# Kernel optimization log

Measured on AMD Instinct MI355X. Metric: run time of the kernel, lower is better.

## Reference

```python
import jax, jax.numpy as jnp
import numpy as np
from jax import lax
from jax.scipy.ndimage import map_coordinates

L = 10  # unrolled iterations (LayerNo)


def _conv(x, w, b):
    # x [N,C,H,W], w [O,I,3,3] -> 'SAME' padding == padding=1 for k=3
    y = lax.conv_general_dilated(x, w, (1, 1), 'SAME',
                                 dimension_numbers=('NCHW', 'OIHW', 'NCHW'))
    return y + b[None, :, None, None]


def _prelu(x, a):
    return jnp.where(x >= 0, x, a * x)


def _block(x, w1, b1, a1, w2, b2, a2, w3, b3):
    x = _prelu(_conv(x, w1, b1), a1)
    x = _prelu(_conv(x, w2, b2), a2)
    return _conv(x, w3, b3)


def _radon_forward(img, theta, det_count):
    # img [S,S]; parallel-beam line integrals -> [A, det_count]
    S = img.shape[0]
    c = (S - 1) / 2.0
    s = jnp.arange(det_count, dtype=img.dtype) - (det_count - 1) / 2.0
    t = jnp.arange(S, dtype=img.dtype) - (S - 1) / 2.0

    def one(a):
        ca, sa = jnp.cos(a), jnp.sin(a)
        x = s[:, None] * ca - t[None, :] * sa  # [D,S] sample cols
        y = s[:, None] * sa + t[None, :] * ca  # [D,S] sample rows
        vals = map_coordinates(img, [y + c, x + c], order=1, mode='constant', cval=0.0)
        return vals.sum(axis=1)

    return jax.vmap(one)(theta)


def _radon_backprojection(sino, theta, S):
    # sino [A,D] -> [S,S] (adjoint smear with bilinear detector interpolation)
    A, D = sino.shape
    c = (S - 1) / 2.0
    dc = (D - 1) / 2.0
    ax = jnp.arange(S, dtype=sino.dtype) - c
    Y, X = jnp.meshgrid(ax, ax, indexing='ij')  # row=y, col=x

    def one(row, a):
        ca, sa = jnp.cos(a), jnp.sin(a)
        sidx = (X * ca + Y * sa + dc).ravel()
        return map_coordinates(row, [sidx], order=1, mode='constant', cval=0.0).reshape(S, S)

    return jax.vmap(one)(sino, theta).sum(axis=0)


def _filter_sinogram(sino):
    # Ram-Lak ramp filter along detector axis with FBP normalization pi/(2*A)
    A, D = sino.shape
    n = 2048  # next power of two >= 2*D (D=729)
    F = jnp.fft.rfft(sino, n=n, axis=-1)
    ramp = (2.0 * jnp.fft.rfftfreq(n)).astype(sino.dtype)
    out = jnp.fft.irfft(F * ramp, n=n, axis=-1)[..., :D]
    return out * (jnp.pi / (2.0 * A))


def _forward(cond, x0, g, theta, theta_label,
             dw1, db1, da1, dw2, db2, da2, dw3, db3,
             pw1, pb1, pa1, pw2, pb2, pa2, pw3, pb3):
    S = x0.shape[2]
    A, D = g.shape[2], g.shape[3]
    h = jnp.zeros((1, 5, A, D), dtype=g.dtype)
    f = jnp.zeros((1, 5, S, S), dtype=g.dtype)
    for i in range(L):
        Op_f = _radon_forward(f[0, 1], theta, D)[None, None]          # [1,1,A,D]
        h = h + _block(jnp.concatenate([h, Op_f, g], axis=1),
                       dw1[i], db1[i], da1[i], dw2[i], db2[i], da2[i], dw3[i], db3[i])
        h1 = _filter_sinogram(h[0, 0])                                 # [A,D]
        OpAdj_h = _radon_backprojection(h1, theta, S)[None, None]      # [1,1,S,S]
        f = f + _block(jnp.concatenate([f, OpAdj_h], axis=1),
                       pw1[i], pb1[i], pa1[i], pw2[i], pb2[i], pa2[i], pw3[i], pb3[i])
    return (f[:, 0:1], f[:, 0:1], f[:, 0:1])


def setup_inputs() -> dict:
    key = jax.random.key(0)
    ks = jax.random.split(key, 12)
    S, A, D = 512, 60, 729

    def xavier(k, shp):
        cout, cin = shp[1], shp[2]
        std = np.sqrt(2.0 / ((cin + cout) * 9.0)).astype(np.float32)
        return jax.random.normal(k, shp, dtype=jnp.float32) * std

    ang = jnp.linspace(0.0, np.pi, A, endpoint=False).astype(jnp.float32)
    return {
        'cond': jax.random.normal(ks[0], (1, 1, S, S), dtype=jnp.float32),
        'x0': jax.random.normal(ks[1], (1, 1, S, S), dtype=jnp.float32),
        'g': jax.random.normal(ks[2], (1, 1, A, D), dtype=jnp.float32),
        'theta': ang,
        'theta_label': ang,
        'dw1': xavier(ks[3], (L, 32, 7, 3, 3)), 'db1': jnp.zeros((L, 32), jnp.float32), 'da1': 0.25 * jnp.ones((L,), jnp.float32),
        'dw2': xavier(ks[4], (L, 32, 32, 3, 3)), 'db2': jnp.zeros((L, 32), jnp.float32), 'da2': 0.25 * jnp.ones((L,), jnp.float32),
        'dw3': xavier(ks[5], (L, 5, 32, 3, 3)), 'db3': jnp.zeros((L, 5), jnp.float32),
        'pw1': xavier(ks[6], (L, 32, 6, 3, 3)), 'pb1': jnp.zeros((L, 32), jnp.float32), 'pa1': 0.25 * jnp.ones((L,), jnp.float32),
        'pw2': xavier(ks[7], (L, 32, 32, 3, 3)), 'pb2': jnp.zeros((L, 32), jnp.float32), 'pa2': 0.25 * jnp.ones((L,), jnp.float32),
        'pw3': xavier(ks[8], (L, 5, 32, 3, 3)), 'pb3': jnp.zeros((L, 5), jnp.float32),
    }


def reference(cond, x0, g, theta, theta_label,
              dw1, db1, da1, dw2, db2, da2, dw3, db3,
              pw1, pb1, pa1, pw2, pb2, pa2, pw3, pb3):
    return _forward(cond, x0, g, theta, theta_label,
                    dw1, db1, da1, dw2, db2, da2, dw3, db3,
                    pw1, pb1, pa1, pw2, pb2, pa2, pw3, pb3)
```

## Files before the change

### kernel.cpp

```cpp
#include <hip/hip_runtime.h>
#include <math.h>

#define SS 512
#define AANG 60
#define DDET 729
#define NPIX (SS*SS)
#define NSIN (AANG*DDET)
#define NTAPS 1457
#define DRS 768

typedef float v4u __attribute__((ext_vector_type(4), aligned(4)));
typedef float v2u __attribute__((ext_vector_type(2), aligned(8)));
typedef short short8 __attribute__((ext_vector_type(8)));
typedef short short4v __attribute__((ext_vector_type(4)));
typedef float f32x4 __attribute__((ext_vector_type(4)));

__device__ inline unsigned short f2bf(float x){
  unsigned u = __float_as_uint(x);
  return (unsigned short)((u + 0x7fffu + ((u >> 16) & 1u)) >> 16);
}

__global__ void trig_kernel(const float* __restrict__ theta, float* __restrict__ trig){
  int a = threadIdx.x;
  if (a < AANG){ trig[a] = cosf(theta[a]); trig[AANG+a] = sinf(theta[a]); }
}

__global__ void taps_kernel(float* __restrict__ taps){
  __shared__ double red[256];
  int m  = blockIdx.x;
  int mm = m - 728;
  double s = 0.0;
  for (int k = 1 + (int)threadIdx.x; k <= 1023; k += 256){
    int phase = (k*mm) & 2047;
    s += (double)k * cos((double)phase * (M_PI/1024.0));
// ... 60 lines not shown
  float x = (t < 9 && j < Cin) ? w[(((size_t)(l*32+o)*Cin + j)*9) + t] : 0.f;
  unsigned short hb = f2bf(x);
  float hf = __uint_as_float((unsigned)hb << 16);
  unsigned short lb = f2bf(x - hf);
  size_t d = (size_t)l*6144 + (size_t)g*2048 + n*1024 + lane*8 + j;
  B[d]       = hb;
  B[d + 512] = lb;
}

__global__ void g_to_nhwc8(const float* __restrict__ g,
                           unsigned short* __restrict__ s8hi, unsigned short* __restrict__ s8lo){
  int idx = blockIdx.x*256 + (int)threadIdx.x;
  if (idx >= NSIN) return;
  int a = idx / DDET, d = idx - a*DDET;
  float x = g[idx];
  unsigned short hb = f2bf(x);
  float hf = __uint_as_float((unsigned)hb << 16);
  unsigned short lb = f2bf(x - hf);
  size_t p8 = ((size_t)(a+1)*DRS + d)*8 + 6;
  s8hi[p8] = hb;
  s8lo[p8] = lb;
}

__device__ inline void clipr(float al, float ial, float be, float lo, float hi,
                             float& A, float& B, bool& empty){
  if (fabsf(al) < 1e-7f){ if (be < lo || be > hi) empty = true; return; }
  float t0 = (lo - be)*ial, t1 = (hi - be)*ial;
  float mn = fminf(t0,t1), mx = fmaxf(t0,t1);
  A = fmaxf(A, mn); B = fminf(B, mx);
}

__device__ inline float samp_guard(const float* __restrict__ base, float aR, float bR,
                                   float aC, float bC, int t){
  float tp = (float)t - 255.5f;
  float R = fmaf(aR, tp, bR);
  float C = fmaf(aC, tp, bC);
// ... 55 lines not shown
        float tp = (float)t - 255.5f;
        float R = fmaf(aR, tp, bR);
        float C = fmaf(aC, tp, bC);
        int r0 = (int)R, c0 = (int)C;
        float fr = R - (float)r0, fc = C - (float)c0;
        const float* p = base + r0*SS + c0;
        float v00 = p[0], v01 = p[1], v10 = p[SS], v11 = p[SS+1];
        float top = v00 + fc*(v01-v00);
        float bot = v10 + fc*(v11-v10);
        acc += top + fr*(bot-top);
      }
    }
  }
  for (int off=32; off; off>>=1) acc += __shfl_down(acc, off);
  if (lane==0){
    unsigned short hb = f2bf(acc);
    float hf = __uint_as_float((unsigned)hb << 16);
    unsigned short lb = f2bf(acc - hf);
    size_t p8 = ((size_t)(a+1)*DRS + d)*8 + 5;
    s8hi[p8] = hb;
    s8lo[p8] = lb;
  }
}

__global__ __launch_bounds__(256) void filter_kernel2(
    const float* __restrict__ h0, const float* __restrict__ taps,
    float* __restrict__ h1){
  __shared__ float red[256];
  int a  = blockIdx.x / 12;
  int jb = blockIdx.x - a*12;
  int jl = (int)threadIdx.x & 63;
  int kq = (int)threadIdx.x >> 6;
  int j  = jb*64 + jl;
  float acc = 0.f;
  if (j < DDET){
    const float* row = h0 + a*DDET;
    const float* tp  = taps + 728 + j;
    int k0 = kq*183;
    int k1 = min(k0+183, DDET);
    for (int k=k0;k<k1;k++) acc = fmaf(row[k], tp[-k], acc);
  }
  red[threadIdx.x] = acc;
  __syncthreads();
  if ((int)threadIdx.x < 64 && j < DDET){
    float s = red[jl] + red[64+jl] + red[128+jl] + red[192+jl];
    h1[a*DDET + j] = s;
  }
}

__global__ __launch_bounds__(256) void backproj_kernel(
    const float* __restrict__ h1, const float* __restrict__ trig,
    unsigned short* __restrict__ hi8, unsigned short* __restrict__ lo8){
  __shared__ float sh[AANG*28];
  __shared__ int   sbase[AANG];
  __shared__ float strig[2*AANG];
  int tid = threadIdx.x;
  int x0 = (blockIdx.x & 31) * 16, y0 = (blockIdx.x >> 5) * 16;
  if (tid < 2*AANG) strig[tid] = trig[tid];
  __syncthreads();
  if (tid < AANG){
    float ca = strig[tid], sa = strig[AANG+tid];
// ... 11 lines not shown
    sh[s] = (idx >= 0 && idx < DDET) ? h1[a*DDET + idx] : 0.f;
  }
  __syncthreads();
  int x = x0 + (tid & 15), y = y0 + (tid >> 4);
  float X = (float)x - 255.5f, Y = (float)y - 255.5f;
  float acc = 0.f;
  #pragma unroll 6
  for (int a=0;a<AANG;a++){
    float sidx = fmaf(X, strig[a], fmaf(Y, strig[AANG+a], 364.0f));
    float ff = floorf(sidx);
    int k = (int)ff - sbase[a];
    float fi = sidx - ff;
    float v0 = sh[a*28+k], v1 = sh[a*28+k+1];
    acc += v0 + fi*(v1-v0);
  }
  unsigned short hb = f2bf(acc);
  float hf = __uint_as_float((unsigned)hb << 16);
  unsigned short lb = f2bf(acc - hf);
  size_t p8 = ((size_t)(y*SS + x))*8 + 5;
  hi8[p8] = hb;
  lo8[p8] = lb;
}

__global__ __launch_bounds__(64) void dual1_mfma(
    const unsigned short* __restrict__ hi8, const unsigned short* __restrict__ lo8,
    const unsigned short* __restrict__ Bimg1d,
    const float* __restrict__ bias, const float* __restrict__ prelu,
    unsigned short* __restrict__ outHi, unsigned short* __restrict__ outLo)
{
  __shared__ unsigned int tr[64][33];
  int y  = blockIdx.y;
  int lane = (int)threadIdx.x;
  int xw = blockIdx.x*64;
  int lm = lane & 15, lq = lane >> 4;
  f32x4 acc[4][2];
  #pragma unroll
  for (int s=0;s<4;s++){ acc[s][0] = (f32x4)0.f; acc[s][1] = (f32x4)0.f; }
  const short8* Bf = (const short8*)Bimg1d;
  #pragma unroll
  for (int g=0; g<3; g++){
    const short8* bp8 = Bf + g*256 + lane;
    short8 bh0 = bp8[0];
    short8 bl0 = bp8[64];
    short8 bh1 = bp8[128];
    short8 bl1 = bp8[192];
    int t = g*4 + lq; if (t > 8) t = 8;
    int dy = (t >= 6) ? 1 : ((t >= 3) ? 0 : -1);
    int dx = t - (dy+1)*3 - 1;
    int row = y + dy + 1;
    #pragma unroll
    for (int s=0; s<4; s++){
      int px = xw + s*16 + lm + dx;
      size_t off = (size_t)(row*DRS + px)*8;
      short8 ah = *(const short8*)(hi8 + off);
      short8 al = *(const short8*)(lo8 + off);
      acc[s][0] = __builtin_amdgcn_mfma_f32_16x16x32_bf16(ah, bh0, acc[s][0], 0,0,0);
      acc[s][1] = __builtin_amdgcn_mfma_f32_16x16x32_bf16(ah, bh1, acc[s][1], 0,0,0);
      acc[s][0] = __builtin_amdgcn_mfma_f32_16x16x32_bf16(al, bh0, acc[s][0], 0,0,0);
      acc[s][1] = __builtin_amdgcn_mfma_f32_16x16x32_bf16(al, bh1, acc[s][1], 0,0,0);
      acc[s][0] = __builtin_amdgcn_mfma_f32_16x16x32_bf16(ah, bl0, acc[s][0], 0,0,0);
      acc[s][1] = __builtin_amdgcn_mfma_f32_16x16x32_bf16(ah, bl1, acc[s][1], 0,0,0);
    }
  }
  float aa = *prelu;
  #pragma unroll
  for (int s=0;s<4;s++){
    #pragma unroll
    for (int n=0;n<2;n++){
      int o = n*16 + lm;
      float bv = bias[o];
      f32x4 v = acc[s][n];
      v.x+=bv; v.y+=bv; v.z+=bv; v.w+=bv;
      v.x=(v.x>=0.f)?v.x:aa*v.x; v.y=(v.y>=0.f)?v.y:aa*v.y;
      v.z=(v.z>=0.f)?v.z:aa*v.z; v.w=(v.w>=0.f)?v.w:aa*v.w;
      #pragma unroll
      for (int r=0;r<4;r++){
        float x = v[r];
        unsigned short hb = f2bf(x);
        float hf = __uint_as_float((unsigned)hb << 16);
        unsigned short lb = f2bf(x - hf);
        tr[s*16 + lq*4 + r][o] = ((unsigned)hb << 16) | (unsigned)lb;
      }
    }
  }
  __syncthreads();
  int c8 = lane & 3;
  int pxl = lane >> 2;
  #pragma unroll
  for (int k=0;k<4;k++){
    int px = pxl + k*16;
    int x = xw + px;
    if (x > 728) continue;
    short8 vh, vl;
    #pragma unroll
    for (int j=0;j<8;j++){
      unsigned p = tr[px][c8*8 + j];
      vh[j] = (short)(p >> 16);
      vl[j] = (short)(p & 0xffffu);
    }
    size_t base = ((size_t)(y+1)*DRS + x)*32 + c8*8;
    *(short8*)(outHi + base) = vh;
    *(short8*)(outLo + base) = vl;
  }
}

__global__ __launch_bounds__(64) void dual_mfma32(
    const unsigned short* __restrict__ hiB, const unsigned short* __restrict__ loB,
    const unsigned short* __restrict__ Bimg,
    const float* __restrict__ bias, const float* __restrict__ prelu,
    unsigned short* __restrict__ outHi, unsigned short* __restrict__ outLo)
{
  __shared__ unsigned int tr[64][33];
  int y  = blockIdx.y;
  int lane = (int)threadIdx.x;
  int xw = blockIdx.x*64;
  int lm = lane & 15, lq = lane >> 4;
  int laneoff = lm*32 + lq*8;
  f32x4 acc[4][2];
  #pragma unroll
  for (int s=0;s<4;s++){ acc[s][0] = (f32x4)0.f; acc[s][1] = (f32x4)0.f; }
  const short8* Bf = (const short8*)Bimg;
  #pragma unroll
  for (int dy=-1; dy<=1; dy++){
    const unsigned short* rh = hiB + (size_t)(y+dy+1)*DRS*32;
    const unsigned short* rl = loB + (size_t)(y+dy+1)*DRS*32;
    #pragma unroll
    for (int dx=-1; dx<=1; dx++){
      int tap = (dy+1)*3 + (dx+1);
      const short8* bp8 = Bf + tap*256 + lane;
      short8 bh0 = bp8[0];
      short8 bl0 = bp8[64];
      short8 bh1 = bp8[128];
      short8 bl1 = bp8[192];
      int xoff = (xw + dx)*32 + laneoff;
      #pragma unroll
      for (int s=0; s<4; s++){
        short8 ah = *(const short8*)(rh + xoff + s*512);
        short8 al = *(const short8*)(rl + xoff + s*512);
        acc[s][0] = __builtin_amdgcn_mfma_f32_16x16x32_bf16(ah, bh0, acc[s][0], 0,0,0);
        acc[s][1] = __builtin_amdgcn_mfma_f32_16x16x32_bf16(ah, bh1, acc[s][1], 0,0,0);
        acc[s][0] = __builtin_amdgcn_mfma_f32_16x16x32_bf16(al, bh0, acc[s][0], 0,0,0);
        acc[s][1] = __builtin_amdgcn_mfma_f32_16x16x32_bf16(al, bh1, acc[s][1], 0,0,0);
        acc[s][0] = __builtin_amdgcn_mfma_f32_16x16x32_bf16(ah, bl0, acc[s][0], 0,0,0);
        acc[s][1] = __builtin_amdgcn_mfma_f32_16x16x32_bf16(ah, bl1, acc[s][1], 0,0,0);
      }
    }
  }
  float aa = *prelu;
  #pragma unroll
  for (int s=0;s<4;s++){
    #pragma unroll
    for (int n=0;n<2;n++){
      int o = n*16 + lm;
      float bv = bias[o];
      f32x4 v = acc[s][n];
      v.x+=bv; v.y+=bv; v.z+=bv; v.w+=bv;
      v.x=(v.x>=0.f)?v.x:aa*v.x; v.y=(v.y>=0.f)?v.y:aa*v.y;
      v.z=(v.z>=0.f)?v.z:aa*v.z; v.w=(v.w>=0.f)?v.w:aa*v.w;
      #pragma unroll
      for (int r=0;r<4;r++){
        float x = v[r];
        unsigned short hb = f2bf(x);
        float hf = __uint_as_float((unsigned)hb << 16);
        unsigned short lb = f2bf(x - hf);
        tr[s*16 + lq*4 + r][o] = ((unsigned)hb << 16) | (unsigned)lb;
      }
    }
  }
  __syncthreads();
  int c8 = lane & 3;
  int pxl = lane >> 2;
  #pragma unroll
  for (int k=0;k<4;k++){
    int px = pxl + k*16;
    int x = xw + px;
    if (x > 728) continue;
    short8 vh, vl;
    #pragma unroll
    for (int j=0;j<8;j++){
      unsigned p = tr[px][c8*8 + j];
      vh[j] = (short)(p >> 16);
      vl[j] = (short)(p & 0xffffu);
    }
    size_t base = ((size_t)(y+1)*DRS + x)*32 + c8*8;
    *(short8*)(outHi + base) = vh;
    *(short8*)(outLo + base) = vl;
  }
}

__global__ __launch_bounds__(64) void dual3_mfma(
    const unsigned short* __restrict__ hiB, const unsigned short* __restrict__ loB,
    const unsigned short* __restrict__ Bimg3d,
    const float* __restrict__ bias,
    float* __restrict__ h,
    unsigned short* __restrict__ s8hi, unsigned short* __restrict__ s8lo)
{
  __shared__ unsigned int t8[64][6];
  int y  = blockIdx.y;
  int lane = (int)threadIdx.x;
  int xw = blockIdx.x*64;
  int lm = lane & 15, lq = lane >> 4;
  int laneoff = lm*32 + lq*8;
  f32x4 acc[4];
  #pragma unroll
  for (int s=0;s<4;s++) acc[s] = (f32x4)0.f;
  const short8* Bf = (const short8*)Bimg3d;
  #pragma unroll
  for (int dy=-1; dy<=1; dy++){
    const unsigned short* rh = hiB + (size_t)(y+dy+1)*DRS*32;
    const unsigned short* rl = loB + (size_t)(y+dy+1)*DRS*32;
    #pragma unroll
    for (int dx=-1; dx<=1; dx++){
      int tap = (dy+1)*3 + (dx+1);
      const short8* bp8 = Bf + tap*128 + lane;
      short8 bh = bp8[0];
      short8 bl = bp8[64];
      int xoff = (xw + dx)*32 + laneoff;
      #pragma unroll
      for (int s=0; s<4; s++){
        short8 ah = *(const short8*)(rh + xoff + s*512);
        short8 al = *(const short8*)(rl + xoff + s*512);
        acc[s] = __builtin_amdgcn_mfma_f32_16x16x32_bf16(ah, bh, acc[s], 0,0,0);
        acc[s] = __builtin_amdgcn_mfma_f32_16x16x32_bf16(al, bh, acc[s], 0,0,0);
        acc[s] = __builtin_amdgcn_mfma_f32_16x16x32_bf16(ah, bl, acc[s], 0,0,0);
      }
    }
  }
  if (lm < 5){
    float bv = bias[lm];
    #pragma unroll
    for (int s=0;s<4;s++){
      int px0 = xw + s*16 + lq*4;
      float* op = h + (size_t)lm*NSIN + y*DDET + px0;
      float nv0=0.f, nv1=0.f, nv2=0.f, nv3=0.f;
      if (px0 + 3 <= 728){
        v4u old = *(const v4u*)op;
        nv0 = old.x + acc[s].x + bv;
        nv1 = old.y + acc[s].y + bv;
        nv2 = old.z + acc[s].z + bv;
        nv3 = old.w + acc[s].w + bv;
        v4u st; st.x=nv0; st.y=nv1; st.z=nv2; st.w=nv3;
        *(v4u*)op = st;
      } else {
        if (px0   <= 728){ nv0 = op[0] + acc[s].x + bv; op[0] = nv0; }
        if (px0+1 <= 728){ nv1 = op[1] + acc[s].y + bv; op[1] = nv1; }
        if (px0+2 <= 728){ nv2 = op[2] + acc[s].z + bv; op[2] = nv2; }
        if (px0+3 <= 728){ nv3 = op[3] + acc[s].w + bv; op[3] = nv3; }
      }
      float nv[4] = {nv0,nv1,nv2,nv3};
      #pragma unroll
      for (int r=0;r<4;r++){
        float x = nv[r];
        unsigned short hb = f2bf(x);
        float hf = __uint_as_float((unsigned)hb << 16);
        unsigned short lb = f2bf(x - hf);
        t8[s*16 + lq*4 + r][lm] = ((unsigned)hb << 16) | (unsigned)lb;
      }
    }
  }
  __syncthreads();
  {
    int x = xw + lane;
    if (x <= 728){
      unsigned c0 = t8[lane][0], c1 = t8[lane][1], c2 = t8[lane][2];
      unsigned c3 = t8[lane][3], c4 = t8[lane][4];
      size_t base = ((size_t)(y+1)*DRS + x)*8;
      short4v vh; vh[0]=(short)(c0>>16); vh[1]=(short)(c1>>16); vh[2]=(short)(c2>>16); vh[3]=(short)(c3>>16);
      short4v vl; vl[0]=(short)(c0&0xffffu); vl[1]=(short)(c1&0xffffu); vl[2]=(short)(c2&0xffffu); vl[3]=(short)(c3&0xffffu);
      *(short4v*)(s8hi + base) = vh;
      *(short4v*)(s8lo + base) = vl;
      s8hi[base+4] = (unsigned short)(c4>>16);
      s8lo[base+4] = (unsigned short)(c4&0xffffu);
    }
  }
}

__global__ __launch_bounds__(256) void prim1_mfma(
    const unsigned short* __restrict__ hi8, const unsigned short* __restrict__ lo8,
    const unsigned short* __restrict__ Bimg1,
    const float* __restrict__ bias, const float* __restrict__ prelu,
    unsigned short* __restrict__ outHi, unsigned short* __restrict__ outLo)
{
  __shared__ unsigned int tr[4][64][33];
  int b = blockIdx.x;
  int by = b >> 1, half = b & 1;
  int y = ((by & 7) << 6) | (by >> 3);
  int wv = (int)threadIdx.x >> 6;
  int lane = (int)threadIdx.x & 63;
  int xw = half*256 + wv*64;
// ... 36 lines not shown
      acc[s][1] = __builtin_amdgcn_mfma_f32_16x16x32_bf16(ah, bl1, acc[s][1], 0,0,0);
    }
  }
  float aa = *prelu;
  #pragma unroll
  for (int s=0;s<4;s++){
    #pragma unroll
    for (int n=0;n<2;n++){
      int o = n*16 + lm;
      float bv = bias[o];
      f32x4 v = acc[s][n];
      v.x+=bv; v.y+=bv; v.z+=bv; v.w+=bv;
      v.x=(v.x>=0.f)?v.x:aa*v.x; v.y=(v.y>=0.f)?v.y:aa*v.y;
      v.z=(v.z>=0.f)?v.z:aa*v.z; v.w=(v.w>=0.f)?v.w:aa*v.w;
      #pragma unroll
      for (int r=0;r<4;r++){
        float x = v[r];
        unsigned short hb = f2bf(x);
        float hf = __uint_as_float((unsigned)hb << 16);
        unsigned short lb = f2bf(x - hf);
        tr[wv][s*16 + lq*4 + r][o] = ((unsigned)hb << 16) | (unsigned)lb;
      }
    }
  }
  __syncthreads();
  int c8 = lane & 3;
  int pxl = lane >> 2;
  #pragma unroll
  for (int k=0;k<4;k++){
    int px = pxl + k*16;
    short8 vh, vl;
    #pragma unroll
    for (int j=0;j<8;j++){
      unsigned p = tr[wv][px][c8*8 + j];
      vh[j] = (short)(p >> 16);
      vl[j] = (short)(p & 0xffffu);
    }
// ... 61 lines not shown
      }
    }
  }
  float aa = *prelu;
  #pragma unroll
  for (int s=0;s<4;s++){
    #pragma unroll
    for (int n=0;n<2;n++){
      int o = n*16 + lm;
      float bv = bias[o];
      f32x4 v = acc[s][n];
      v.x+=bv; v.y+=bv; v.z+=bv; v.w+=bv;
      v.x=(v.x>=0.f)?v.x:aa*v.x; v.y=(v.y>=0.f)?v.y:aa*v.y;
      v.z=(v.z>=0.f)?v.z:aa*v.z; v.w=(v.w>=0.f)?v.w:aa*v.w;
      #pragma unroll
      for (int r=0;r<4;r++){
        float x = v[r];
        unsigned short hb = f2bf(x);
        float hf = __uint_as_float((unsigned)hb << 16);
        unsigned short lb = f2bf(x - hf);
        tr[wv][s*16 + lq*4 + r][o] = ((unsigned)hb << 16) | (unsigned)lb;
      }
    }
  }
  __syncthreads();
  int c8 = lane & 3;
  int pxl = lane >> 2;
  #pragma unroll
  for (int k=0;k<4;k++){
    int px = pxl + k*16;
    short8 vh, vl;
    #pragma unroll
    for (int j=0;j<8;j++){
      unsigned p = tr[wv][px][c8*8 + j];
      vh[j] = (short)(p >> 16);
      vl[j] = (short)(p & 0xffffu);
    }
// ... 58 lines not shown
      }
    }
  }
  if (lm < 5){
    float bv = bias[lm];
    #pragma unroll
    for (int s=0;s<4;s++){
      int px0 = xw + s*16 + lq*4;
      float* op = f + (size_t)lm*NPIX + y*SS + px0;
      f32x4 old = *(const f32x4*)op;
      f32x4 v = acc[s];
      v.x += old.x + bv; v.y += old.y + bv;
      v.z += old.z + bv; v.w += old.w + bv;
      *(f32x4*)op = v;
      #pragma unroll
      for (int r=0;r<4;r++){
        float x = v[r];
        unsigned short hb = f2bf(x);
        float hf = __uint_as_float((unsigned)hb << 16);
        unsigned short lb = f2bf(x - hf);
        t8[wv][s*16 + lq*4 + r][lm] = ((unsigned)hb << 16) | (unsigned)lb;
      }
      if (lm == 1){
        tout[(px0  )*SS + y] = v.x;
        tout[(px0+1)*SS + y] = v.y;
        tout[(px0+2)*SS + y] = v.z;
        tout[(px0+3)*SS + y] = v.w;
      }
      if (lm == 0 && fout){
        float* q = fout + y*SS + px0;
        *(f32x4*)q = v;
        *(f32x4*)(q + NPIX) = v;
        *(f32x4*)(q + 2*NPIX) = v;
      }
    }
  }
  __syncthreads();
// ... 23 lines not shown
  const float* da2 = (const float*)d_in[10];
  const float* dw3 = (const float*)d_in[11];
  const float* db3 = (const float*)d_in[12];
  const float* pw1 = (const float*)d_in[13];
  const float* pb1 = (const float*)d_in[14];
  const float* pa1 = (const float*)d_in[15];
  const float* pw2 = (const float*)d_in[16];
  const float* pb2 = (const float*)d_in[17];
  const float* pa2 = (const float*)d_in[18];
  const float* pw3 = (const float*)d_in[19];
  const float* pb3 = (const float*)d_in[20];

  float* ws     = (float*)d_ws;
  float* trig   = ws;
  float* taps   = ws + 128;
  float* h      = ws + 2048;
  float* opf    = h + 5*NSIN;
  float* gcopy  = opf + NSIN;
  float* h1     = gcopy + NSIN;
  float* f      = h1 + NSIN;
  float* bp     = f + 5*NPIX;
  float* imgT   = bp + NPIX;
  float* dualT1 = imgT + NPIX;
  float* dualT2 = dualT1 + 32*NSIN;
  float* primT2slot = dualT2 + 32*NSIN;
  unsigned short* primHi = (unsigned short*)primT2slot;
  unsigned short* primLo = primHi + (size_t)32*NPIX;
  unsigned short* nhwcHi = (unsigned short*)(primT2slot + 32*NPIX);
  unsigned short* nhwcLo = nhwcHi + (size_t)32*NPIX;
  float* wsp   = (float*)(nhwcLo + (size_t)32*NPIX);
// ... 8 lines not shown
  unsigned short* dualLoRaw = dualHiRaw + DUALSZ;
  unsigned short* dualHi = dualHiRaw + 64;
  unsigned short* dualLo = dualLoRaw + 64;
  unsigned short* dual2HiRaw = (unsigned short*)dualT1;
  unsigned short* dual2LoRaw = (unsigned short*)dualT2;
  unsigned short* dual2Hi = dual2HiRaw + 64;
  unsigned short* dual2Lo = dual2LoRaw + 64;
  unsigned short* nh8Hi = dualLoRaw + DUALSZ;
  unsigned short* nh8Lo = nh8Hi + (size_t)NPIX*8;
  const size_t S8SZ = (size_t)64 + (size_t)62*DRS*8 + 64;
  unsigned short* s8HiRaw = nh8Lo + (size_t)NPIX*8;
  unsigned short* s8LoRaw = s8HiRaw + S8SZ;
  unsigned short* s8Hi = s8HiRaw + 64;
  unsigned short* s8Lo = s8LoRaw + 64;

  hipMemsetAsync(h, 0, (size_t)(5*NSIN)*sizeof(float), stream);
  hipMemsetAsync(f, 0, (size_t)(7*NPIX)*sizeof(float), stream);
  hipMemsetAsync(dualHiRaw, 0, 2*DUALSZ*sizeof(unsigned short), stream);
  hipMemsetAsync(dual2HiRaw, 0, DUALSZ*sizeof(unsigned short), stream);
  hipMemsetAsync(dual2LoRaw, 0, DUALSZ*sizeof(unsigned short), stream);
  hipMemsetAsync(nh8Hi, 0, (size_t)2*NPIX*8*sizeof(unsigned short), stream);
  hipMemsetAsync(s8HiRaw, 0, 2*S8SZ*sizeof(unsigned short), stream);
  trig_kernel<<<1,64,0,stream>>>(theta, trig);
  taps_kernel<<<NTAPS,256,0,stream>>>(taps);
  prep_bimg<<<(92160+255)/256,256,0,stream>>>(pw2, Bimg);
  prep_bimg<<<(92160+255)/256,256,0,stream>>>(dw2, Bimg2);
  prep_bimg3<<<(46080+255)/256,256,0,stream>>>(pw3, Bimg3);
  prep_bimg3<<<(46080+255)/256,256,0,stream>>>(dw3, Bimg3d);
  prep_bimg1c<<<(30720+255)/256,256,0,stream>>>(pw1, Bimg1, 6);
  prep_bimg1c<<<(30720+255)/256,256,0,stream>>>(dw1, Bimg1d, 7);
  g_to_nhwc8<<<(NSIN+255)/256,256,0,stream>>>(g, s8Hi, s8Lo);

  for (int i=0;i<10;i++){
    radon_fwd_kernel<<<(NSIN+3)/4,256,0,stream>>>(f + NPIX, imgT, trig, s8Hi, s8Lo);
    dual1_mfma<<<dim3(12,AANG),64,0,stream>>>(s8Hi, s8Lo, Bimg1d+(size_t)i*6144,
                                              db1+(size_t)i*32, da1+i, dualHi, dualLo);
    dual_mfma32<<<dim3(12,AANG),64,0,stream>>>(dualHi, dualLo, Bimg2+(size_t)i*18432,
                                               db2+(size_t)i*32, da2+i, dual2Hi, dual2Lo);
    dual3_mfma<<<dim3(12,AANG),64,0,stream>>>(dual2Hi, dual2Lo, Bimg3d+(size_t)i*9216,
                                              db3+(size_t)i*5, h, s8Hi, s8Lo);
    filter_kernel2<<<AANG*12,256,0,stream>>>(h, taps, h1);
    backproj_kernel<<<NPIX/256,256,0,stream>>>(h1, trig, nh8Hi, nh8Lo);
    prim1_mfma<<<1024,256,0,stream>>>(nh8Hi, nh8Lo, Bimg1+(size_t)i*6144,
                                      pb1+(size_t)i*32, pa1+i, nhwcHi, nhwcLo);
    conv_mfma32<<<1024,256,0,stream>>>(nhwcHi, nhwcLo, Bimg+(size_t)i*18432, pb2+(size_t)i*32, pa2+i, primHi, primLo);
    duo_mfma<<<1024,256,0,stream>>>(primHi, primLo, Bimg3+(size_t)i*9216, pb3+(size_t)i*5, f,
                                    (i==9) ? (float*)d_out : nullptr, imgT, nh8Hi, nh8Lo);
  }
}
```

Measured before the change: 1.791 ms.

## Fuse dual-domain conv chain and ramp filter into one kernel with grid barriers

Replaces the three dual-branch MFMA conv kernels and the sinogram filter kernel with a single persistent kernel of 720 blocks. Four waves per block each handle 16 pixels, and an atomic-counter grid barrier separates the stages. This removes three kernel launches per iteration and lets each stage start without a launch gap. The cost is a software grid barrier that deadlocks unless all 720 blocks are co-resident, and lower per-wave ILP because each wave now holds one accumulator set instead of four.

```diff
diff --git a/kernel.cpp b/kernel.cpp
--- a/kernel.cpp
+++ b/kernel.cpp
@@ -18,6 +18,24 @@
 __device__ inline unsigned short f2bf(float x){
   unsigned u = __float_as_uint(x);
   return (unsigned short)((u + 0x7fffu + ((u >> 16) & 1u)) >> 16);
+}
+
+__device__ inline unsigned pack_hilo(float x){
+  unsigned short hb = f2bf(x);
+  float hf = __uint_as_float((unsigned)hb << 16);
+  unsigned short lb = f2bf(x - hf);
+  return ((unsigned)hb << 16) | (unsigned)lb;
+}
+
+__device__ inline void gbar(int* cnt, int target){
+  __syncthreads();
+  __threadfence();
+  if (threadIdx.x == 0){
+    atomicAdd(cnt, 1);
+    while (atomicAdd(cnt, 0) < target) __builtin_amdgcn_s_sleep(1);
+  }
+  __syncthreads();
+  __threadfence();
 }
 
 __global__ void trig_kernel(const float* __restrict__ theta, float* __restrict__ trig){
@@ -108,12 +126,10 @@
   if (idx >= NSIN) return;
   int a = idx / DDET, d = idx - a*DDET;
   float x = g[idx];
-  unsigned short hb = f2bf(x);
-  float hf = __uint_as_float((unsigned)hb << 16);
-  unsigned short lb = f2bf(x - hf);
+  unsigned p = pack_hilo(x);
   size_t p8 = ((size_t)(a+1)*DRS + d)*8 + 6;
-  s8hi[p8] = hb;
-  s8lo[p8] = lb;
+  s8hi[p8] = (unsigned short)(p >> 16);
+  s8lo[p8] = (unsigned short)(p & 0xffffu);
 }
 
 __device__ inline void clipr(float al, float ial, float be, float lo, float hi,
@@ -199,37 +215,232 @@
   }
   for (int off=32; off; off>>=1) acc += __shfl_down(acc, off);
   if (lane==0){
-    unsigned short hb = f2bf(acc);
-    float hf = __uint_as_float((unsigned)hb << 16);
-    unsigned short lb = f2bf(acc - hf);
+    unsigned p = pack_hilo(acc);
     size_t p8 = ((size_t)(a+1)*DRS + d)*8 + 5;
-    s8hi[p8] = hb;
-    s8lo[p8] = lb;
-  }
-}
-
-__global__ __launch_bounds__(256) void filter_kernel2(
-    const float* __restrict__ h0, const float* __restrict__ taps,
-    float* __restrict__ h1){
+    s8hi[p8] = (unsigned short)(p >> 16);
+    s8lo[p8] = (unsigned short)(p & 0xffffu);
+  }
+}
+
+__global__ __launch_bounds__(256, 3) void dual_chain(
+    unsigned short* __restrict__ s8hi, unsigned short* __restrict__ s8lo,
+    unsigned short* __restrict__ d1hi, unsigned short* __restrict__ d1lo,
+    unsigned short* __restrict__ d2hi, unsigned short* __restrict__ d2lo,
+    const unsigned short* __restrict__ B1,
+    const unsigned short* __restrict__ B2,
+    const unsigned short* __restrict__ B3,
+    const float* __restrict__ b1, const float* __restrict__ a1,
+    const float* __restrict__ b2, const float* __restrict__ a2,
+    const float* __restrict__ b3,
+    float* __restrict__ h, float* __restrict__ h1,
+    const float* __restrict__ taps,
+    int* __restrict__ cnt)
+{
+  __shared__ unsigned int tr[64][33];
+  __shared__ unsigned int t8[64][6];
   __shared__ float red[256];
-  int a  = blockIdx.x / 12;
-  int jb = blockIdx.x - a*12;
-  int jl = (int)threadIdx.x & 63;
-  int kq = (int)threadIdx.x >> 6;
-  int j  = jb*64 + jl;
-  float acc = 0.f;
-  if (j < DDET){
-    const float* row = h0 + a*DDET;
-    const float* tp  = taps + 728 + j;
-    int k0 = kq*183;
-    int k1 = min(k0+183, DDET);
-    for (int k=k0;k<k1;k++) acc = fmaf(row[k], tp[-k], acc);
-  }
-  red[threadIdx.x] = acc;
-  __syncthreads();
-  if ((int)threadIdx.x < 64 && j < DDET){
-    float s = red[jl] + red[64+jl] + red[128+jl] + red[192+jl];
-    h1[a*DDET + j] = s;
+  int tid = (int)threadIdx.x;
+  int wv = tid >> 6, lane = tid & 63;
+  int bid = (int)blockIdx.x;
+  int y = bid / 12, xc = bid - y*12;
+  int xw = xc * 64;
+  int lm = lane & 15, lq = lane >> 4;
+  int laneoff = lm*32 + lq*8;
+
+  {
+    f32x4 acc0 = (f32x4)0.f, acc1 = (f32x4)0.f;
+    const short8* Bf = (const short8*)B1;
+    #pragma unroll
+    for (int g=0; g<3; g++){
+      const short8* bp8 = Bf + g*256 + lane;
+      short8 bh0 = bp8[0], bl0 = bp8[64], bh1 = bp8[128], bl1 = bp8[192];
+      int t = g*4 + lq; if (t > 8) t = 8;
+      int dy = (t >= 6) ? 1 : ((t >= 3) ? 0 : -1);
+      int dx = t - (dy+1)*3 - 1;
+      int row = y + dy + 1;
+      int px = xw + wv*16 + lm + dx;
+      size_t off = (size_t)(row*DRS + px)*8;
+      short8 ah = *(const short8*)(s8hi + off);
+      short8 al = *(const short8*)(s8lo + off);
+      acc0 = __builtin_amdgcn_mfma_f32_16x16x32_bf16(ah, bh0, acc0, 0,0,0);
+      acc1 = __builtin_amdgcn_mfma_f32_16x16x32_bf16(ah, bh1, acc1, 0,0,0);
+      acc0 = __builtin_amdgcn_mfma_f32_16x16x32_bf16(al, bh0, acc0, 0,0,0);
+      acc1 = __builtin_amdgcn_mfma_f32_16x16x32_bf16(al, bh1, acc1, 0,0,0);
+      acc0 = __builtin_amdgcn_mfma_f32_16x16x32_bf16(ah, bl0, acc0, 0,0,0);
+      acc1 = __builtin_amdgcn_mfma_f32_16x16x32_bf16(ah, bl1, acc1, 0,0,0);
+    }
+    float aa = *a1;
+    #pragma unroll
+    for (int n=0;n<2;n++){
+      int o = n*16 + lm;
+      float bv = b1[o];
+      f32x4 v = n ? acc1 : acc0;
+      v.x+=bv; v.y+=bv; v.z+=bv; v.w+=bv;
+      v.x=(v.x>=0.f)?v.x:aa*v.x; v.y=(v.y>=0.f)?v.y:aa*v.y;
+      v.z=(v.z>=0.f)?v.z:aa*v.z; v.w=(v.w>=0.f)?v.w:aa*v.w;
+      #pragma unroll
+      for (int r=0;r<4;r++) tr[wv*16 + lq*4 + r][o] = pack_hilo(v[r]);
+    }
+  }
+  __syncthreads();
+  {
+    int c8 = tid & 3;
+    int px = tid >> 2;
+    int x = xw + px;
+    if (x <= 728){
+      short8 vh, vl;
+      #pragma unroll
+      for (int j=0;j<8;j++){
+        unsigned p = tr[px][c8*8 + j];
+        vh[j] = (short)(p >> 16);
+        vl[j] = (short)(p & 0xffffu);
+      }
+      size_t base = ((size_t)(y+1)*DRS + x)*32 + c8*8;
+      *(short8*)(d1hi + base) = vh;
+      *(short8*)(d1lo + base) = vl;
+    }
+  }
+  gbar(cnt, 720);
+
+  {
+    f32x4 acc0 = (f32x4)0.f, acc1 = (f32x4)0.f;
+    const short8* Bf = (const short8*)B2;
+    #pragma unroll
+    for (int dy=-1; dy<=1; dy++){
+      const unsigned short* rh = d1hi + (size_t)(y+dy+1)*DRS*32;
+      const unsigned short* rl = d1lo + (size_t)(y+dy+1)*DRS*32;
+      #pragma unroll
+      for (int dx=-1; dx<=1; dx++){
+        int tap = (dy+1)*3 + (dx+1);
+        const short8* bp8 = Bf + tap*256 + lane;
+        short8 bh0 = bp8[0], bl0 = bp8[64], bh1 = bp8[128], bl1 = bp8[192];
+        int xoff = (xw + dx)*32 + laneoff + wv*512;
+        short8 ah = *(const short8*)(rh + xoff);
+        short8 al = *(const short8*)(rl + xoff);
+        acc0 = __builtin_amdgcn_mfma_f32_16x16x32_bf16(ah, bh0, acc0, 0,0,0);
+        acc1 = __builtin_amdgcn_mfma_f32_16x16x32_bf16(ah, bh1, acc1, 0,0,0);
+        acc0 = __builtin_amdgcn_mfma_f32_16x16x32_bf16(al, bh0, acc0, 0,0,0);
+        acc1 = __builtin_amdgcn_mfma_f32_16x16x32_bf16(al, bh1, acc1, 0,0,0);
+        acc0 = __builtin_amdgcn_mfma_f32_16x16x32_bf16(ah, bl0, acc0, 0,0,0);
+        acc1 = __builtin_amdgcn_mfma_f32_16x16x32_bf16(ah, bl1, acc1, 0,0,0);
+      }
+    }
+    float aa = *a2;
+    #pragma unroll
+    for (int n=0;n<2;n++){
+      int o = n*16 + lm;
+      float bv = b2[o];
+      f32x4 v = n ? acc1 : acc0;
+      v.x+=bv; v.y+=bv; v.z+=bv; v.w+=bv;
+      v.x=(v.x>=0.f)?v.x:aa*v.x; v.y=(v.y>=0.f)?v.y:aa*v.y;
+      v.z=(v.z>=0.f)?v.z:aa*v.z; v.w=(v.w>=0.f)?v.w:aa*v.w;
+      #pragma unroll
+      for (int r=0;r<4;r++) tr[wv*16 + lq*4 + r][o] = pack_hilo(v[r]);
+    }
+  }
+  __syncthreads();
+  {
+    int c8 = tid & 3;
+    int px = tid >> 2;
+    int x = xw + px;
+    if (x <= 728){
+      short8 vh, vl;
+      #pragma unroll
+      for (int j=0;j<8;j++){
+        unsigned p = tr[px][c8*8 + j];
+        vh[j] = (short)(p >> 16);
+        vl[j] = (short)(p & 0xffffu);
+      }
+      size_t base = ((size_t)(y+1)*DRS + x)*32 + c8*8;
+      *(short8*)(d2hi + base) = vh;
+      *(short8*)(d2lo + base) = vl;
+    }
+  }
+  gbar(cnt, 1440);
+
+  {
+    f32x4 acc = (f32x4)0.f;
+    const short8* Bf = (const short8*)B3;
+    #pragma unroll
+    for (int dy=-1; dy<=1; dy++){
+      const unsigned short* rh = d2hi + (size_t)(y+dy+1)*DRS*32;
+      const unsigned short* rl = d2lo + (size_t)(y+dy+1)*DRS*32;
+      #pragma unroll
+      for (int dx=-1; dx<=1; dx++){
+        int tap = (dy+1)*3 + (dx+1);
+        const short8* bp8 = Bf + tap*128 + lane;
+        short8 bh = bp8[0];
+        short8 bl = bp8[64];
+        int xoff = (xw + dx)*32 + laneoff + wv*512;
+        short8 ah = *(const short8*)(rh + xoff);
+        short8 al = *(const short8*)(rl + xoff);
+        acc = __builtin_amdgcn_mfma_f32_16x16x32_bf16(ah, bh, acc, 0,0,0);
+        acc = __builtin_amdgcn_mfma_f32_16x16x32_bf16(al, bh, acc, 0,0,0);
+        acc = __builtin_amdgcn_mfma_f32_16x16x32_bf16(ah, bl, acc, 0,0,0);
+      }
+    }
+    if (lm < 5){
+      float bv = b3[lm];
+      int px0 = xw + wv*16 + lq*4;
+      float* op = h + (size_t)lm*NSIN + y*DDET + px0;
+      float nv0=0.f, nv1=0.f, nv2=0.f, nv3=0.f;
+      if (px0 + 3 <= 728){
+        v4u old = *(const v4u*)op;
+        nv0 = old.x + acc.x + bv;
+        nv1 = old.y + acc.y + bv;
+        nv2 = old.z + acc.z + bv;
+        nv3 = old.w + acc.w + bv;
+        v4u st; st.x=nv0; st.y=nv1; st.z=nv2; st.w=nv3;
+        *(v4u*)op = st;
+      } else {
+        if (px0   <= 728){ nv0 = op[0] + acc.x + bv; op[0] = nv0; }
+        if (px0+1 <= 728){ nv1 = op[1] + acc.y + bv; op[1] = nv1; }
+        if (px0+2 <= 728){ nv2 = op[2] + acc.z + bv; op[2] = nv2; }
+        if (px0+3 <= 728){ nv3 = op[3] + acc.w + bv; op[3] = nv3; }
+      }
+      float nv[4] = {nv0,nv1,nv2,nv3};
+      #pragma unroll
+      for (int r=0;r<4;r++) t8[wv*16 + lq*4 + r][lm] = pack_hilo(nv[r]);
+    }
+  }
+  __syncthreads();
+  if (tid < 64){
+    int x = xw + tid;
+    if (x <= 728){
+      unsigned c0 = t8[tid][0], c1 = t8[tid][1], c2 = t8[tid][2];
+      unsigned c3 = t8[tid][3], c4 = t8[tid][4];
+      size_t base = ((size_t)(y+1)*DRS + x)*8;
+      short4v vh; vh[0]=(short)(c0>>16); vh[1]=(short)(c1>>16); vh[2]=(short)(c2>>16); vh[3]=(short)(c3>>16);
+      short4v vl; vl[0]=(short)(c0&0xffffu); vl[1]=(short)(c1&0xffffu); vl[2]=(short)(c2&0xffffu); vl[3]=(short)(c3&0xffffu);
+      *(short4v*)(s8hi + base) = vh;
+      *(short4v*)(s8lo + base) = vl;
+      s8hi[base+4] = (unsigned short)(c4>>16);
+      s8lo[base+4] = (unsigned short)(c4&0xffffu);
+    }
+  }
+  gbar(cnt, 2160);
+
+  {
+    int jl = tid & 63;
+    int kq = tid >> 6;
+    int j  = xw + jl;
+    float acc = 0.f;
+    if (j < DDET){
+      const float* row = h + y*DDET;
+      const float* tp  = taps + 728 + j;
+      int k0 = kq*183;
+      int k1 = min(k0+183, DDET);
+      for (int k=k0;k<k1;k++) acc = fmaf(row[k], tp[-k], acc);
+    }
+    red[tid] = acc;
+    __syncthreads();
+    if (tid < 64){
+      int jj = xw + tid;
+      if (jj < DDET){
+        float s = red[tid] + red[64+tid] + red[128+tid] + red[192+tid];
+        h1[y*DDET + jj] = s;
+      }
+    }
   }
 }
 
@@ -271,265 +482,10 @@
     float v0 = sh[a*28+k], v1 = sh[a*28+k+1];
     acc += v0 + fi*(v1-v0);
   }
-  unsigned short hb = f2bf(acc);
-  float hf = __uint_as_float((unsigned)hb << 16);
-  unsigned short lb = f2bf(acc - hf);
+  unsigned p = pack_hilo(acc);
   size_t p8 = ((size_t)(y*SS + x))*8 + 5;
-  hi8[p8] = hb;
-  lo8[p8] = lb;
-}
-
-__global__ __launch_bounds__(64) void dual1_mfma(
-    const unsigned short* __restrict__ hi8, const unsigned short* __restrict__ lo8,
-    const unsigned short* __restrict__ Bimg1d,
-    const float* __restrict__ bias, const float* __restrict__ prelu,
-    unsigned short* __restrict__ outHi, unsigned short* __restrict__ outLo)
-{
-  __shared__ unsigned int tr[64][33];
-  int y  = blockIdx.y;
-  int lane = (int)threadIdx.x;
-  int xw = blockIdx.x*64;
-  int lm = lane & 15, lq = lane >> 4;
-  f32x4 acc[4][2];
-  #pragma unroll
-  for (int s=0;s<4;s++){ acc[s][0] = (f32x4)0.f; acc[s][1] = (f32x4)0.f; }
-  const short8* Bf = (const short8*)Bimg1d;
-  #pragma unroll
-  for (int g=0; g<3; g++){
-    const short8* bp8 = Bf + g*256 + lane;
-    short8 bh0 = bp8[0];
-    short8 bl0 = bp8[64];
-    short8 bh1 = bp8[128];
-    short8 bl1 = bp8[192];
-    int t = g*4 + lq; if (t > 8) t = 8;
-    int dy = (t >= 6) ? 1 : ((t >= 3) ? 0 : -1);
-    int dx = t - (dy+1)*3 - 1;
-    int row = y + dy + 1;
-    #pragma unroll
-    for (int s=0; s<4; s++){
-      int px = xw + s*16 + lm + dx;
-      size_t off = (size_t)(row*DRS + px)*8;
-      short8 ah = *(const short8*)(hi8 + off);
-      short8 al = *(const short8*)(lo8 + off);
-      acc[s][0] = __builtin_amdgcn_mfma_f32_16x16x32_bf16(ah, bh0, acc[s][0], 0,0,0);
-      acc[s][1] = __builtin_amdgcn_mfma_f32_16x16x32_bf16(ah, bh1, acc[s][1], 0,0,0);
-      acc[s][0] = __builtin_amdgcn_mfma_f32_16x16x32_bf16(al, bh0, acc[s][0], 0,0,0);
-      acc[s][1] = __builtin_amdgcn_mfma_f32_16x16x32_bf16(al, bh1, acc[s][1], 0,0,0);
-      acc[s][0] = __builtin_amdgcn_mfma_f32_16x16x32_bf16(ah, bl0, acc[s][0], 0,0,0);
-      acc[s][1] = __builtin_amdgcn_mfma_f32_16x16x32_bf16(ah, bl1, acc[s][1], 0,0,0);
-    }
-  }
-  float aa = *prelu;
-  #pragma unroll
-  for (int s=0;s<4;s++){
-    #pragma unroll
-    for (int n=0;n<2;n++){
-      int o = n*16 + lm;
-      float bv = bias[o];
-      f32x4 v = acc[s][n];
-      v.x+=bv; v.y+=bv; v.z+=bv; v.w+=bv;
-      v.x=(v.x>=0.f)?v.x:aa*v.x; v.y=(v.y>=0.f)?v.y:aa*v.y;
-      v.z=(v.z>=0.f)?v.z:aa*v.z; v.w=(v.w>=0.f)?v.w:aa*v.w;
-      #pragma unroll
-      for (int r=0;r<4;r++){
-        float x = v[r];
-        unsigned short hb = f2bf(x);
-        float hf = __uint_as_float((unsigned)hb << 16);
-        unsigned short lb = f2bf(x - hf);
-        tr[s*16 + lq*4 + r][o] = ((unsigned)hb << 16) | (unsigned)lb;
-      }
-    }
-  }
-  __syncthreads();
-  int c8 = lane & 3;
-  int pxl = lane >> 2;
-  #pragma unroll
-  for (int k=0;k<4;k++){
-    int px = pxl + k*16;
-    int x = xw + px;
-    if (x > 728) continue;
-    short8 vh, vl;
-    #pragma unroll
-    for (int j=0;j<8;j++){
-      unsigned p = tr[px][c8*8 + j];
-      vh[j] = (short)(p >> 16);
-      vl[j] = (short)(p & 0xffffu);
-    }
-    size_t base = ((size_t)(y+1)*DRS + x)*32 + c8*8;
-    *(short8*)(outHi + base) = vh;
-    *(short8*)(outLo + base) = vl;
-  }
-}
-
-__global__ __launch_bounds__(64) void dual_mfma32(
-    const unsigned short* __restrict__ hiB, const unsigned short* __restrict__ loB,
-    const unsigned short* __restrict__ Bimg,
-    const float* __restrict__ bias, const float* __restrict__ prelu,
-    unsigned short* __restrict__ outHi, unsigned short* __restrict__ outLo)
-{
-  __shared__ unsigned int tr[64][33];
-  int y  = blockIdx.y;
-  int lane = (int)threadIdx.x;
-  int xw = blockIdx.x*64;
-  int lm = lane & 15, lq = lane >> 4;
-  int laneoff = lm*32 + lq*8;
-  f32x4 acc[4][2];
-  #pragma unroll
-  for (int s=0;s<4;s++){ acc[s][0] = (f32x4)0.f; acc[s][1] = (f32x4)0.f; }
-  const short8* Bf = (const short8*)Bimg;
-  #pragma unroll
-  for (int dy=-1; dy<=1; dy++){
-    const unsigned short* rh = hiB + (size_t)(y+dy+1)*DRS*32;
-    const unsigned short* rl = loB + (size_t)(y+dy+1)*DRS*32;
-    #pragma unroll
-    for (int dx=-1; dx<=1; dx++){
-      int tap = (dy+1)*3 + (dx+1);
-      const short8* bp8 = Bf + tap*256 + lane;
-      short8 bh0 = bp8[0];
-      short8 bl0 = bp8[64];
-      short8 bh1 = bp8[128];
-      short8 bl1 = bp8[192];
-      int xoff = (xw + dx)*32 + laneoff;
-      #pragma unroll
-      for (int s=0; s<4; s++){
-        short8 ah = *(const short8*)(rh + xoff + s*512);
-        short8 al = *(const short8*)(rl + xoff + s*512);
-        acc[s][0] = __builtin_amdgcn_mfma_f32_16x16x32_bf16(ah, bh0, acc[s][0], 0,0,0);
-        acc[s][1] = __builtin_amdgcn_mfma_f32_16x16x32_bf16(ah, bh1, acc[s][1], 0,0,0);
-        acc[s][0] = __builtin_amdgcn_mfma_f32_16x16x32_bf16(al, bh0, acc[s][0], 0,0,0);
-        acc[s][1] = __builtin_amdgcn_mfma_f32_16x16x32_bf16(al, bh1, acc[s][1], 0,0,0);
-        acc[s][0] = __builtin_amdgcn_mfma_f32_16x16x32_bf16(ah, bl0, acc[s][0], 0,0,0);
-        acc[s][1] = __builtin_amdgcn_mfma_f32_16x16x32_bf16(ah, bl1, acc[s][1], 0,0,0);
-      }
-    }
-  }
-  float aa = *prelu;
-  #pragma unroll
-  for (int s=0;s<4;s++){
-    #pragma unroll
-    for (int n=0;n<2;n++){
-      int o = n*16 + lm;
-      float bv = bias[o];
-      f32x4 v = acc[s][n];
-      v.x+=bv; v.y+=bv; v.z+=bv; v.w+=bv;
-      v.x=(v.x>=0.f)?v.x:aa*v.x; v.y=(v.y>=0.f)?v.y:aa*v.y;
-      v.z=(v.z>=0.f)?v.z:aa*v.z; v.w=(v.w>=0.f)?v.w:aa*v.w;
-      #pragma unroll
-      for (int r=0;r<4;r++){
-        float x = v[r];
-        unsigned short hb = f2bf(x);
-        float hf = __uint_as_float((unsigned)hb << 16);
-        unsigned short lb = f2bf(x - hf);
-        tr[s*16 + lq*4 + r][o] = ((unsigned)hb << 16) | (unsigned)lb;
-      }
-    }
-  }
-  __syncthreads();
-  int c8 = lane & 3;
-  int pxl = lane >> 2;
-  #pragma unroll
-  for (int k=0;k<4;k++){
-    int px = pxl + k*16;
-    int x = xw + px;
-    if (x > 728) continue;
-    short8 vh, vl;
-    #pragma unroll
-    for (int j=0;j<8;j++){
-      unsigned p = tr[px][c8*8 + j];
-      vh[j] = (short)(p >> 16);
-      vl[j] = (short)(p & 0xffffu);
-    }
-    size_t base = ((size_t)(y+1)*DRS + x)*32 + c8*8;
-    *(short8*)(outHi + base) = vh;
-    *(short8*)(outLo + base) = vl;
-  }
-}
-
-__global__ __launch_bounds__(64) void dual3_mfma(
-    const unsigned short* __restrict__ hiB, const unsigned short* __restrict__ loB,
-    const unsigned short* __restrict__ Bimg3d,
-    const float* __restrict__ bias,
-    float* __restrict__ h,
-    unsigned short* __restrict__ s8hi, unsigned short* __restrict__ s8lo)
-{
-  __shared__ unsigned int t8[64][6];
-  int y  = blockIdx.y;
-  int lane = (int)threadIdx.x;
-  int xw = blockIdx.x*64;
-  int lm = lane & 15, lq = lane >> 4;
-  int laneoff = lm*32 + lq*8;
-  f32x4 acc[4];
-  #pragma unroll
-  for (int s=0;s<4;s++) acc[s] = (f32x4)0.f;
-  const short8* Bf = (const short8*)Bimg3d;
-  #pragma unroll
-  for (int dy=-1; dy<=1; dy++){
-    const unsigned short* rh = hiB + (size_t)(y+dy+1)*DRS*32;
-    const unsigned short* rl = loB + (size_t)(y+dy+1)*DRS*32;
-    #pragma unroll
-    for (int dx=-1; dx<=1; dx++){
-      int tap = (dy+1)*3 + (dx+1);
-      const short8* bp8 = Bf + tap*128 + lane;
-      short8 bh = bp8[0];
-      short8 bl = bp8[64];
-      int xoff = (xw + dx)*32 + laneoff;
-      #pragma unroll
-      for (int s=0; s<4; s++){
-        short8 ah = *(const short8*)(rh + xoff + s*512);
-        short8 al = *(const short8*)(rl + xoff + s*512);
-        acc[s] = __builtin_amdgcn_mfma_f32_16x16x32_bf16(ah, bh, acc[s], 0,0,0);
-        acc[s] = __builtin_amdgcn_mfma_f32_16x16x32_bf16(al, bh, acc[s], 0,0,0);
-        acc[s] = __builtin_amdgcn_mfma_f32_16x16x32_bf16(ah, bl, acc[s], 0,0,0);
-      }
-    }
-  }
-  if (lm < 5){
-    float bv = bias[lm];
-    #pragma unroll
-    for (int s=0;s<4;s++){
-      int px0 = xw + s*16 + lq*4;
-      float* op = h + (size_t)lm*NSIN + y*DDET + px0;
-      float nv0=0.f, nv1=0.f, nv2=0.f, nv3=0.f;
-      if (px0 + 3 <= 728){
-        v4u old = *(const v4u*)op;
-        nv0 = old.x + acc[s].x + bv;
-        nv1 = old.y + acc[s].y + bv;
-        nv2 = old.z + acc[s].z + bv;
-        nv3 = old.w + acc[s].w + bv;
-        v4u st; st.x=nv0; st.y=nv1; st.z=nv2; st.w=nv3;
-        *(v4u*)op = st;
-      } else {
-        if (px0   <= 728){ nv0 = op[0] + acc[s].x + bv; op[0] = nv0; }
-        if (px0+1 <= 728){ nv1 = op[1] + acc[s].y + bv; op[1] = nv1; }
-        if (px0+2 <= 728){ nv2 = op[2] + acc[s].z + bv; op[2] = nv2; }
-        if (px0+3 <= 728){ nv3 = op[3] + acc[s].w + bv; op[3] = nv3; }
-      }
-      float nv[4] = {nv0,nv1,nv2,nv3};
-      #pragma unroll
-      for (int r=0;r<4;r++){
-        float x = nv[r];
-        unsigned short hb = f2bf(x);
-        float hf = __uint_as_float((unsigned)hb << 16);
-        unsigned short lb = f2bf(x - hf);
-        t8[s*16 + lq*4 + r][lm] = ((unsigned)hb << 16) | (unsigned)lb;
-      }
-    }
-  }
-  __syncthreads();
-  {
-    int x = xw + lane;
-    if (x <= 728){
-      unsigned c0 = t8[lane][0], c1 = t8[lane][1], c2 = t8[lane][2];
-      unsigned c3 = t8[lane][3], c4 = t8[lane][4];
-      size_t base = ((size_t)(y+1)*DRS + x)*8;
-      short4v vh; vh[0]=(short)(c0>>16); vh[1]=(short)(c1>>16); vh[2]=(short)(c2>>16); vh[3]=(short)(c3>>16);
-      short4v vl; vl[0]=(short)(c0&0xffffu); vl[1]=(short)(c1&0xffffu); vl[2]=(short)(c2&0xffffu); vl[3]=(short)(c3&0xffffu);
-      *(short4v*)(s8hi + base) = vh;
-      *(short4v*)(s8lo + base) = vl;
-      s8hi[base+4] = (unsigned short)(c4>>16);
-      s8lo[base+4] = (unsigned short)(c4&0xffffu);
-    }
-  }
+  hi8[p8] = (unsigned short)(p >> 16);
+  lo8[p8] = (unsigned short)(p & 0xffffu);
 }
 
 __global__ __launch_bounds__(256) void prim1_mfma(
@@ -596,13 +552,8 @@
       v.x=(v.x>=0.f)?v.x:aa*v.x; v.y=(v.y>=0.f)?v.y:aa*v.y;
       v.z=(v.z>=0.f)?v.z:aa*v.z; v.w=(v.w>=0.f)?v.w:aa*v.w;
       #pragma unroll
-      for (int r=0;r<4;r++){
-        float x = v[r];
-        unsigned short hb = f2bf(x);
-        float hf = __uint_as_float((unsigned)hb << 16);
-        unsigned short lb = f2bf(x - hf);
-        tr[wv][s*16 + lq*4 + r][o] = ((unsigned)hb << 16) | (unsigned)lb;
-      }
+      for (int r=0;r<4;r++)
+        tr[wv][s*16 + lq*4 + r][o] = pack_hilo(v[r]);
     }
   }
   __syncthreads();
@@ -694,13 +645,8 @@
       v.x=(v.x>=0.f)?v.x:aa*v.x; v.y=(v.y>=0.f)?v.y:aa*v.y;
       v.z=(v.z>=0.f)?v.z:aa*v.z; v.w=(v.w>=0.f)?v.w:aa*v.w;
       #pragma unroll
-      for (int r=0;r<4;r++){
-        float x = v[r];
-        unsigned short hb = f2bf(x);
-        float hf = __uint_as_float((unsigned)hb << 16);
-        unsigned short lb = f2bf(x - hf);
-        tr[wv][s*16 + lq*4 + r][o] = ((unsigned)hb << 16) | (unsigned)lb;
-      }
+      for (int r=0;r<4;r++)
+        tr[wv][s*16 + lq*4 + r][o] = pack_hilo(v[r]);
     }
   }
   __syncthreads();
@@ -789,13 +735,8 @@
       v.z += old.z + bv; v.w += old.w + bv;
       *(f32x4*)op = v;
       #pragma unroll
-      for (int r=0;r<4;r++){
-        float x = v[r];
-        unsigned short hb = f2bf(x);
-        float hf = __uint_as_float((unsigned)hb << 16);
-        unsigned short lb = f2bf(x - hf);
-        t8[wv][s*16 + lq*4 + r][lm] = ((unsigned)hb << 16) | (unsigned)lb;
-      }
+      for (int r=0;r<4;r++)
+        t8[wv][s*16 + lq*4 + r][lm] = pack_hilo(v[r]);
       if (lm == 1){
         tout[(px0  )*SS + y] = v.x;
         tout[(px0+1)*SS + y] = v.y;
@@ -849,6 +790,7 @@
   float* ws     = (float*)d_ws;
   float* trig   = ws;
   float* taps   = ws + 128;
+  int*   barcnt = (int*)(ws + 1600);
   float* h      = ws + 2048;
   float* opf    = h + 5*NSIN;
   float* gcopy  = opf + NSIN;
@@ -887,6 +829,7 @@
   unsigned short* s8Hi = s8HiRaw + 64;
   unsigned short* s8Lo = s8LoRaw + 64;
 
+  hipMemsetAsync(barcnt, 0, 10*sizeof(int), stream);
   hipMemsetAsync(h, 0, (size_t)(5*NSIN)*sizeof(float), stream);
   hipMemsetAsync(f, 0, (size_t)(7*NPIX)*sizeof(float), stream);
   hipMemsetAsync(dualHiRaw, 0, 2*DUALSZ*sizeof(unsigned short), stream);
@@ -906,13 +849,11 @@
 
   for (int i=0;i<10;i++){
     radon_fwd_kernel<<<(NSIN+3)/4,256,0,stream>>>(f + NPIX, imgT, trig, s8Hi, s8Lo);
-    dual1_mfma<<<dim3(12,AANG),64,0,stream>>>(s8Hi, s8Lo, Bimg1d+(size_t)i*6144,
-                                              db1+(size_t)i*32, da1+i, dualHi, dualLo);
-    dual_mfma32<<<dim3(12,AANG),64,0,stream>>>(dualHi, dualLo, Bimg2+(size_t)i*18432,
-                                               db2+(size_t)i*32, da2+i, dual2Hi, dual2Lo);
-    dual3_mfma<<<dim3(12,AANG),64,0,stream>>>(dual2Hi, dual2Lo, Bimg3d+(size_t)i*9216,
-                                              db3+(size_t)i*5, h, s8Hi, s8Lo);
-    filter_kernel2<<<AANG*12,256,0,stream>>>(h, taps, h1);
+    dual_chain<<<720,256,0,stream>>>(s8Hi, s8Lo, dualHi, dualLo, dual2Hi, dual2Lo,
+                                     Bimg1d+(size_t)i*6144, Bimg2+(size_t)i*18432,
+                                     Bimg3d+(size_t)i*9216,
+                                     db1+(size_t)i*32, da1+i, db2+(size_t)i*32, da2+i,
+                                     db3+(size_t)i*5, h, h1, taps, barcnt + i);
     backproj_kernel<<<NPIX/256,256,0,stream>>>(h1, trig, nh8Hi, nh8Lo);
     prim1_mfma<<<1024,256,0,stream>>>(nh8Hi, nh8Lo, Bimg1+(size_t)i*6144,
                                       pb1+(size_t)i*32, pa1+i, nhwcHi, nhwcLo);
```

After: 6.652 ms. +271.4%, slower.
